# Optimization experiments

Hardware: AMD Instinct MI355X
Metric: run time of the kernel (lower is better)

The kernel has to match this reference:

```python
import jax, jax.numpy as jnp
import numpy as np

DT = 3600.0  # Euler step size (seconds)
N = 2_097_152  # number of timesteps = len(t)


def _get_AB(params):
    """Build the 3x3 A and 3x5 B RC-network matrices from the 7 parameters."""
    Cai, Cwe, Cwi, Re, Ri, Rw, Rg = (params[i] for i in range(7))
    z = jnp.zeros((), params.dtype)
    A = jnp.stack([
        jnp.stack([-1.0 / Cai * (1.0 / Rg + 1.0 / Ri), z, 1.0 / (Cai * Ri)]),
        jnp.stack([z, -1.0 / Cwe * (1.0 / Re + 1.0 / Rw), 1.0 / (Cwe * Rw)]),
        jnp.stack([1.0 / (Cwi * Ri), 1.0 / (Cwi * Rw), -1.0 / Cwi * (1.0 / Rw + 1.0 / Ri)]),
    ])  # [3,3]
    B = jnp.stack([
        jnp.stack([1.0 / (Cai * Rg), 1.0 / Cai, 1.0 / Cai, z, z]),
        jnp.stack([1.0 / (Cwe * Re), z, z, 1.0 / Cwe, z]),
        jnp.stack([z, z, z, z, 1.0 / Cwi]),
    ])  # [3,5]
    return A, B


def setup_inputs() -> dict:
    key = jax.random.key(0)
    d = jax.random.normal(key, (N, 5), dtype=jnp.float32)  # disturbance inputs per step
    params = jnp.array([100000.0, 30000.0, 300000.0, 10.0, 1.0, 10.0, 10.0], dtype=jnp.float32)
    x0 = jnp.array([20.0, 30.0, 26.0], dtype=jnp.float32)  # initial state temps
    return {"params": params, "x0": x0, "d": d}


def reference(params, x0, d):
    # One explicit-Euler step per timestep:
    #   x_{i+1} = x_i + dt*(A x_i + B d_i) = M x_i + c_i,  M = I + dt*A, c_i = dt*B d_i
    A, B = _get_AB(params)
    M = jnp.eye(3, dtype=params.dtype) + DT * A  # [3,3]
    c = DT * (d[:-1] @ B.T)  # [N-1,3]; last row of d is unused (loop runs len(t)-1 steps)

    def step(x, ci):
        xn = M @ x + ci
        return xn, xn

    _, xs = jax.lax.scan(step, x0, c)  # xs: [N-1,3]
    return jnp.concatenate([x0[None, :], xs], axis=0)  # [N,3] == x_all
```

## Files before the change

### kernel.cpp

```cpp
#include <hip/hip_runtime.h>


static constexpr int  N_T   = 2097152;
static constexpr long STEPS = N_T - 1;
static constexpr int  SEG   = 16;
static constexpr int  NSEG  = 131072;
static constexpr int  BLK   = 256;
static constexpr int  NBLK  = NSEG / BLK;

struct Coef {
    float m00,m02,m11,m12,m20,m21,m22;
    float b00,b01,b10,b13,b24;
};

__device__ __forceinline__ Coef derive(const float* __restrict__ p){
    Coef o;
    const float dt = 3600.0f;
    float Cai=p[0],Cwe=p[1],Cwi=p[2],Re=p[3],Ri=p[4],Rw=p[5],Rg=p[6];
    o.m00 = 1.0f + dt * (-1.0f/Cai*(1.0f/Rg + 1.0f/Ri));
    o.m02 = dt * (1.0f/(Cai*Ri));
    o.m11 = 1.0f + dt * (-1.0f/Cwe*(1.0f/Re + 1.0f/Rw));
    o.m12 = dt * (1.0f/(Cwe*Rw));
    o.m20 = dt * (1.0f/(Cwi*Ri));
    o.m21 = dt * (1.0f/(Cwi*Rw));
    o.m22 = 1.0f + dt * (-1.0f/Cwi*(1.0f/Rw + 1.0f/Ri));
    o.b00 = dt * (1.0f/(Cai*Rg));
    o.b01 = dt * (1.0f/Cai);
    o.b10 = dt * (1.0f/(Cwe*Re));
    o.b13 = dt * (1.0f/Cwe);
    o.b24 = dt * (1.0f/Cwi);
    return o;
}

__device__ __forceinline__ void step(const Coef& C, float& s0, float& s1, float& s2,
                                     float d0, float d1, float d2, float d3, float d4){
    float c0 = fmaf(C.b00, d0, C.b01*(d1+d2));
    float c1 = fmaf(C.b10, d0, C.b13*d3);
    float c2 = C.b24*d4;
    float n0 = fmaf(C.m00, s0, fmaf(C.m02, s2, c0));
    float n1 = fmaf(C.m11, s1, fmaf(C.m12, s2, c1));
    float n2 = fmaf(C.m20, s0, fmaf(C.m21, s1, fmaf(C.m22, s2, c2)));
    s0=n0; s1=n1; s2=n2;
}

__device__ __forceinline__ void mm3(const double* X, const double* Y, double* Z){
    #pragma unroll
    for (int r=0;r<3;++r){
        #pragma unroll
        for (int c=0;c<3;++c){
            Z[r*3+c] = X[r*3+0]*Y[0*3+c] + X[r*3+1]*Y[1*3+c] + X[r*3+2]*Y[2*3+c];
        }
    }
}

__device__ __forceinline__ void msq(double* X){
    double T[9]; mm3(X,X,T);
    #pragma unroll
    for (int i=0;i<9;++i) X[i]=T[i];
}

__device__ __forceinline__ void computeM(const float* __restrict__ p, double* Md){
    double Cai=p[0],Cwe=p[1],Cwi=p[2],Re=p[3],Ri=p[4],Rw=p[5],Rg=p[6];
    const double dt = 3600.0;
    Md[0]=1.0 - dt*((1.0/Rg + 1.0/Ri)/Cai); Md[1]=0.0;                              Md[2]=dt/(Cai*Ri);
    Md[3]=0.0;                              Md[4]=1.0 - dt*((1.0/Re + 1.0/Rw)/Cwe); Md[5]=dt/(Cwe*Rw);
    Md[6]=dt/(Cwi*Ri);                      Md[7]=dt/(Cwi*Rw);                      Md[8]=1.0 - dt*((1.0/Rw + 1.0/Ri)/Cwi);
}

__device__ __forceinline__ void lds_scan(float* Ish, int t, int nthr,
                                         double* Qd, float& v0, float& v1, float& v2){
    Ish[t*3+0]=v0; Ish[t*3+1]=v1; Ish[t*3+2]=v2;
    for (int o=1;o<nthr;o<<=1){
        float Qf[9];
        #pragma unroll
        for (int i=0;i<9;++i) Qf[i]=(float)Qd[i];
        __syncthreads();
        float y0=0.f,y1=0.f,y2=0.f;
        if (t>=o){ y0=Ish[(t-o)*3+0]; y1=Ish[(t-o)*3+1]; y2=Ish[(t-o)*3+2]; }
        __syncthreads();
        if (t>=o){
            v0 = Qf[0]*y0+Qf[1]*y1+Qf[2]*y2 + v0;
            v1 = Qf[3]*y0+Qf[4]*y1+Qf[5]*y2 + v1;
            v2 = Qf[6]*y0+Qf[7]*y1+Qf[8]*y2 + v2;
            Ish[t*3+0]=v0; Ish[t*3+1]=v1; Ish[t*3+2]=v2;
        }
        msq(Qd);
    }
    __syncthreads();
}

__global__ __launch_bounds__(256) void k_pass1(const float* __restrict__ d,
                                               const float* __restrict__ p,
                                               float* __restrict__ sArr,
                                               float* __restrict__ blkSum){
    int t = threadIdx.x, b = blockIdx.x;
    int k = b*BLK + t;
    Coef C = derive(p);
    float s0=0.f, s1=0.f, s2=0.f;
    long i0 = (long)k*SEG;
    if (k != NSEG-1){
        const float4* dp = (const float4*)(d + i0*5);
        #pragma unroll
        for (int g=0; g<SEG/4; ++g){
            float4 q0=dp[g*5+0], q1=dp[g*5+1], q2=dp[g*5+2], q3=dp[g*5+3], q4=dp[g*5+4];
            step(C,s0,s1,s2, q0.x,q0.y,q0.z,q0.w,q1.x);
            step(C,s0,s1,s2, q1.y,q1.z,q1.w,q2.x,q2.y);
            step(C,s0,s1,s2, q2.z,q2.w,q3.x,q3.y,q3.z);
            step(C,s0,s1,s2, q3.w,q4.x,q4.y,q4.z,q4.w);
        }
    } else {
        for (long i=i0; i<STEPS; ++i){
            const float* r = d + i*5;
            step(C,s0,s1,s2, r[0],r[1],r[2],r[3],r[4]);
        }
    }
    sArr[k*3+0]=s0; sArr[k*3+1]=s1; sArr[k*3+2]=s2;

    __shared__ float Ish[BLK*3];
    double Pd[9]; computeM(p, Pd);
    msq(Pd); msq(Pd); msq(Pd); msq(Pd);
    double Qd[9];
    #pragma unroll
    for (int i=0;i<9;++i) Qd[i]=Pd[i];
    float v0=s0, v1=s1, v2=s2;
    lds_scan(Ish, t, BLK, Qd, v0, v1, v2);
    if (t==BLK-1){ blkSum[b*3+0]=v0; blkSum[b*3+1]=v1; blkSum[b*3+2]=v2; }
}

__global__ __launch_bounds__(512) void k_pass2(const float* __restrict__ p,
                                               const float* __restrict__ x0,
                                               const float* __restrict__ blkSum,
                                               float* __restrict__ carry){
    __shared__ float Ish[NBLK*3];
    int t = threadIdx.x;
    double Rd[9]; computeM(p, Rd);
    #pragma unroll
    for (int i=0;i<12;++i) msq(Rd);
    float x00=x0[0], x01=x0[1], x02=x0[2];
    float v0=blkSum[t*3+0], v1=blkSum[t*3+1], v2=blkSum[t*3+2];
    if (t==0){
        float Rf[9];
        #pragma unroll
        for (int i=0;i<9;++i) Rf[i]=(float)Rd[i];
        v0 += Rf[0]*x00+Rf[1]*x01+Rf[2]*x02;
        v1 += Rf[3]*x00+Rf[4]*x01+Rf[5]*x02;
        v2 += Rf[6]*x00+Rf[7]*x01+Rf[8]*x02;
    }
    double Qd[9];
    #pragma unroll
    for (int i=0;i<9;++i) Qd[i]=Rd[i];
    lds_scan(Ish, t, NBLK, Qd, v0, v1, v2);
    if (t==0){ carry[0]=x00; carry[1]=x01; carry[2]=x02; }
    else     { carry[t*3+0]=Ish[(t-1)*3+0]; carry[t*3+1]=Ish[(t-1)*3+1]; carry[t*3+2]=Ish[(t-1)*3+2]; }
}

__global__ __launch_bounds__(256) void k_pass3(const float* __restrict__ d,
                                               const float* __restrict__ p,
                                               const float* __restrict__ sArr,
                                               const float* __restrict__ carry,
                                               const float* __restrict__ x0,
                                               float* __restrict__ out){
    int t = threadIdx.x, b = blockIdx.x;
    int k = b*BLK + t;
    Coef C = derive(p);

    __shared__ float Ish[BLK*3];
    double Pd[9]; computeM(p, Pd);
    msq(Pd); msq(Pd); msq(Pd); msq(Pd);
    float U0=carry[b*3+0], U1=carry[b*3+1], U2=carry[b*3+2];
    float v0=sArr[k*3+0], v1=sArr[k*3+1], v2=sArr[k*3+2];
    if (t==0){
        float Pf[9];
        #pragma unroll
        for (int i=0;i<9;++i) Pf[i]=(float)Pd[i];
        v0 += Pf[0]*U0+Pf[1]*U1+Pf[2]*U2;
        v1 += Pf[3]*U0+Pf[4]*U1+Pf[5]*U2;
        v2 += Pf[6]*U0+Pf[7]*U1+Pf[8]*U2;
    }
    double Qd[9];
    #pragma unroll
    for (int i=0;i<9;++i) Qd[i]=Pd[i];
    lds_scan(Ish, t, BLK, Qd, v0, v1, v2);

    float s0,s1,s2;
    if (t==0){ s0=U0; s1=U1; s2=U2; }
    else     { s0=Ish[(t-1)*3+0]; s1=Ish[(t-1)*3+1]; s2=Ish[(t-1)*3+2]; }

    long i0 = (long)k*SEG;
    if (k==0){ out[0]=x0[0]; out[1]=x0[1]; out[2]=x0[2]; }
    if (k != NSEG-1){
        const float4* dp = (const float4*)(d + i0*5);
        float* op = out + (i0+1)*3;
        #pragma unroll
        for (int g=0; g<SEG/4; ++g){
            float4 q0=dp[g*5+0], q1=dp[g*5+1], q2=dp[g*5+2], q3=dp[g*5+3], q4=dp[g*5+4];
            step(C,s0,s1,s2, q0.x,q0.y,q0.z,q0.w,q1.x);
            op[(g*4+0)*3+0]=s0; op[(g*4+0)*3+1]=s1; op[(g*4+0)*3+2]=s2;
            step(C,s0,s1,s2, q1.y,q1.z,q1.w,q2.x,q2.y);
            op[(g*4+1)*3+0]=s0; op[(g*4+1)*3+1]=s1; op[(g*4+1)*3+2]=s2;
            step(C,s0,s1,s2, q2.z,q2.w,q3.x,q3.y,q3.z);
            op[(g*4+2)*3+0]=s0; op[(g*4+2)*3+1]=s1; op[(g*4+2)*3+2]=s2;
            step(C,s0,s1,s2, q3.w,q4.x,q4.y,q4.z,q4.w);
            op[(g*4+3)*3+0]=s0; op[(g*4+3)*3+1]=s1; op[(g*4+3)*3+2]=s2;
        }
    } else {
        for (long i=i0; i<STEPS; ++i){
            const float* r = d + i*5;
            step(C,s0,s1,s2, r[0],r[1],r[2],r[3],r[4]);
            out[(i+1)*3+0]=s0; out[(i+1)*3+1]=s1; out[(i+1)*3+2]=s2;
        }
    }
}

extern "C" void kernel_launch(void* const* d_in, const int* in_sizes, int n_in,
                              void* d_out, int out_size, void* d_ws, size_t ws_size,
                              hipStream_t stream) {
    const float* params = (const float*)d_in[0];
    const float* x0     = (const float*)d_in[1];
    const float* d      = (const float*)d_in[2];
    float* out    = (float*)d_out;
    float* sArr   = (float*)d_ws;
    float* blkSum = sArr + (size_t)NSEG*3;
    float* carry  = blkSum + (size_t)NBLK*3;

    k_pass1<<<NBLK, BLK, 0, stream>>>(d, params, sArr, blkSum);
    k_pass2<<<1, NBLK, 0, stream>>>(params, x0, blkSum, carry);
    k_pass3<<<NBLK, BLK, 0, stream>>>(d, params, sArr, carry, x0, out);
}
```

Before: 49.72 us.

## Restructure linear-recurrence scan into two kernels with recompute and redundant block-prefix

Replaces the three-pass scan (per-segment sums, single-block carry scan, apply) with two kernels. The first computes only block totals through a tree reduction, and no per-segment state is stored. The second has every block redundantly scan all block totals in LDS to get its own carry, then recomputes its segment sums from the input and does the local scan and output. Segment length drops to 8 and the grid grows to 1024 blocks. This removes the single-block middle launch and the workspace round trip, at the cost of reading the input twice plus redundant per-block carry work.

```diff
diff --git a/kernel.cpp b/kernel.cpp
--- a/kernel.cpp
+++ b/kernel.cpp
@@ -1,12 +1,11 @@
 #include <hip/hip_runtime.h>
 
 
-static constexpr int  N_T   = 2097152;
-static constexpr long STEPS = N_T - 1;
-static constexpr int  SEG   = 16;
-static constexpr int  NSEG  = 131072;
-static constexpr int  BLK   = 256;
-static constexpr int  NBLK  = NSEG / BLK;
+static constexpr long STEPS = 2097151;
+static constexpr int  SEG   = 8;
+static constexpr int  TPB   = 256;
+static constexpr int  NBLK  = 1024;
+static constexpr long NSEGT = (long)NBLK*TPB;
 
 struct Coef {
     float m00,m02,m11,m12,m20,m21,m22;
@@ -45,19 +44,14 @@
 
 __device__ __forceinline__ void mm3(const double* X, const double* Y, double* Z){
     #pragma unroll
-    for (int r=0;r<3;++r){
+    for (int r=0;r<3;++r)
         #pragma unroll
-        for (int c=0;c<3;++c){
+        for (int c=0;c<3;++c)
             Z[r*3+c] = X[r*3+0]*Y[0*3+c] + X[r*3+1]*Y[1*3+c] + X[r*3+2]*Y[2*3+c];
-        }
-    }
-}
-
-__device__ __forceinline__ void msq(double* X){
-    double T[9]; mm3(X,X,T);
-    #pragma unroll
-    for (int i=0;i<9;++i) X[i]=T[i];
-}
+}
+__device__ __forceinline__ void msq(double* X){ double T[9]; mm3(X,X,T);
+    #pragma unroll
+    for (int i=0;i<9;++i) X[i]=T[i]; }
 
 __device__ __forceinline__ void computeM(const float* __restrict__ p, double* Md){
     double Cai=p[0],Cwe=p[1],Cwi=p[2],Re=p[3],Ri=p[4],Rw=p[5],Rg=p[6];
@@ -67,148 +61,180 @@
     Md[6]=dt/(Cwi*Ri);                      Md[7]=dt/(Cwi*Rw);                      Md[8]=1.0 - dt*((1.0/Rw + 1.0/Ri)/Cwi);
 }
 
-__device__ __forceinline__ void lds_scan(float* Ish, int t, int nthr,
-                                         double* Qd, float& v0, float& v1, float& v2){
-    Ish[t*3+0]=v0; Ish[t*3+1]=v1; Ish[t*3+2]=v2;
-    for (int o=1;o<nthr;o<<=1){
+__device__ __forceinline__ void seg_sum(const float* __restrict__ d, long i0, const Coef& C,
+                                        float& s0, float& s1, float& s2){
+    const float4* dp = (const float4*)(d + i0*5);
+    s0=0.f; s1=0.f; s2=0.f;
+    #pragma unroll
+    for (int g=0; g<2; ++g){
+        float4 q0=dp[g*5+0], q1=dp[g*5+1], q2=dp[g*5+2], q3=dp[g*5+3], q4=dp[g*5+4];
+        step(C,s0,s1,s2, q0.x,q0.y,q0.z,q0.w,q1.x);
+        step(C,s0,s1,s2, q1.y,q1.z,q1.w,q2.x,q2.y);
+        step(C,s0,s1,s2, q2.z,q2.w,q3.x,q3.y,q3.z);
+        step(C,s0,s1,s2, q3.w,q4.x,q4.y,q4.z,q4.w);
+    }
+}
+
+__global__ __launch_bounds__(256) void k_tot(const float* __restrict__ d,
+                                             const float* __restrict__ p,
+                                             float* __restrict__ blkTot){
+    int t = threadIdx.x, b = blockIdx.x;
+    long k = (long)b*TPB + t;
+    Coef C = derive(p);
+    float s0,s1,s2;
+    seg_sum(d, k*SEG, C, s0,s1,s2);
+
+    __shared__ float a[TPB*3];
+    a[t*3+0]=s0; a[t*3+1]=s1; a[t*3+2]=s2;
+    double Qd[9]; computeM(p, Qd);
+    msq(Qd); msq(Qd); msq(Qd);
+    __syncthreads();
+    for (int off=1; off<TPB; off<<=1){
         float Qf[9];
         #pragma unroll
         for (int i=0;i<9;++i) Qf[i]=(float)Qd[i];
-        __syncthreads();
+        if ((t & (2*off-1))==0){
+            float l0=a[t*3+0], l1=a[t*3+1], l2=a[t*3+2];
+            float r0=a[(t+off)*3+0], r1=a[(t+off)*3+1], r2=a[(t+off)*3+2];
+            a[t*3+0] = r0 + Qf[0]*l0+Qf[1]*l1+Qf[2]*l2;
+            a[t*3+1] = r1 + Qf[3]*l0+Qf[4]*l1+Qf[5]*l2;
+            a[t*3+2] = r2 + Qf[6]*l0+Qf[7]*l1+Qf[8]*l2;
+        }
+        msq(Qd);
+        __syncthreads();
+    }
+    if (t==0){ blkTot[b*3+0]=a[0]; blkTot[b*3+1]=a[1]; blkTot[b*3+2]=a[2]; }
+}
+
+__global__ __launch_bounds__(256) void k_scan(const float* __restrict__ d,
+                                              const float* __restrict__ p,
+                                              const float* __restrict__ blkTot,
+                                              const float* __restrict__ x0,
+                                              float* __restrict__ out){
+    __shared__ float Tl[NBLK*3];
+    __shared__ float Wl[TPB*3];
+    __shared__ float Sl[TPB*3];
+    __shared__ float powA[8][9];
+    __shared__ float powB[8][9];
+    __shared__ float Rm[9];
+
+    int t = threadIdx.x, b = blockIdx.x;
+    long k = (long)b*TPB + t;
+    long i0 = k*SEG;
+    Coef C = derive(p);
+
+    for (int i=t; i<NBLK*3; i+=TPB) Tl[i] = blkTot[i];
+
+    if (t==0){
+        double Qd[9]; computeM(p, Qd);
+        msq(Qd); msq(Qd); msq(Qd);
+        for (int l=0;l<8;++l){
+            #pragma unroll
+            for (int i=0;i<9;++i) powA[l][i]=(float)Qd[i];
+            msq(Qd);
+        }
+        #pragma unroll
+        for (int i=0;i<9;++i) Rm[i]=(float)Qd[i];
+        msq(Qd); msq(Qd);
+        for (int l=0;l<8;++l){
+            #pragma unroll
+            for (int i=0;i<9;++i) powB[l][i]=(float)Qd[i];
+            msq(Qd);
+        }
+    }
+    __syncthreads();
+
+    float x00=x0[0], x01=x0[1], x02=x0[2];
+    if (t==0){
+        Tl[0] += Rm[0]*x00+Rm[1]*x01+Rm[2]*x02;
+        Tl[1] += Rm[3]*x00+Rm[4]*x01+Rm[5]*x02;
+        Tl[2] += Rm[6]*x00+Rm[7]*x01+Rm[8]*x02;
+    }
+    __syncthreads();
+
+    float w0=Tl[(4*t)*3+0], w1=Tl[(4*t)*3+1], w2=Tl[(4*t)*3+2];
+    #pragma unroll
+    for (int j=1;j<4;++j){
+        float n0 = Tl[(4*t+j)*3+0] + Rm[0]*w0+Rm[1]*w1+Rm[2]*w2;
+        float n1 = Tl[(4*t+j)*3+1] + Rm[3]*w0+Rm[4]*w1+Rm[5]*w2;
+        float n2 = Tl[(4*t+j)*3+2] + Rm[6]*w0+Rm[7]*w1+Rm[8]*w2;
+        w0=n0; w1=n1; w2=n2;
+    }
+    Wl[t*3+0]=w0; Wl[t*3+1]=w1; Wl[t*3+2]=w2;
+    __syncthreads();
+    for (int l=0;l<8;++l){
+        int off = 1<<l;
         float y0=0.f,y1=0.f,y2=0.f;
-        if (t>=o){ y0=Ish[(t-o)*3+0]; y1=Ish[(t-o)*3+1]; y2=Ish[(t-o)*3+2]; }
-        __syncthreads();
-        if (t>=o){
-            v0 = Qf[0]*y0+Qf[1]*y1+Qf[2]*y2 + v0;
-            v1 = Qf[3]*y0+Qf[4]*y1+Qf[5]*y2 + v1;
-            v2 = Qf[6]*y0+Qf[7]*y1+Qf[8]*y2 + v2;
-            Ish[t*3+0]=v0; Ish[t*3+1]=v1; Ish[t*3+2]=v2;
-        }
-        msq(Qd);
-    }
-    __syncthreads();
-}
-
-__global__ __launch_bounds__(256) void k_pass1(const float* __restrict__ d,
-                                               const float* __restrict__ p,
-                                               float* __restrict__ sArr,
-                                               float* __restrict__ blkSum){
-    int t = threadIdx.x, b = blockIdx.x;
-    int k = b*BLK + t;
-    Coef C = derive(p);
-    float s0=0.f, s1=0.f, s2=0.f;
-    long i0 = (long)k*SEG;
-    if (k != NSEG-1){
-        const float4* dp = (const float4*)(d + i0*5);
-        #pragma unroll
-        for (int g=0; g<SEG/4; ++g){
-            float4 q0=dp[g*5+0], q1=dp[g*5+1], q2=dp[g*5+2], q3=dp[g*5+3], q4=dp[g*5+4];
-            step(C,s0,s1,s2, q0.x,q0.y,q0.z,q0.w,q1.x);
-            step(C,s0,s1,s2, q1.y,q1.z,q1.w,q2.x,q2.y);
-            step(C,s0,s1,s2, q2.z,q2.w,q3.x,q3.y,q3.z);
-            step(C,s0,s1,s2, q3.w,q4.x,q4.y,q4.z,q4.w);
-        }
-    } else {
-        for (long i=i0; i<STEPS; ++i){
-            const float* r = d + i*5;
-            step(C,s0,s1,s2, r[0],r[1],r[2],r[3],r[4]);
-        }
-    }
-    sArr[k*3+0]=s0; sArr[k*3+1]=s1; sArr[k*3+2]=s2;
-
-    __shared__ float Ish[BLK*3];
-    double Pd[9]; computeM(p, Pd);
-    msq(Pd); msq(Pd); msq(Pd); msq(Pd);
-    double Qd[9];
-    #pragma unroll
-    for (int i=0;i<9;++i) Qd[i]=Pd[i];
+        if (t>=off){ y0=Wl[(t-off)*3+0]; y1=Wl[(t-off)*3+1]; y2=Wl[(t-off)*3+2]; }
+        __syncthreads();
+        if (t>=off){
+            w0 += powB[l][0]*y0+powB[l][1]*y1+powB[l][2]*y2;
+            w1 += powB[l][3]*y0+powB[l][4]*y1+powB[l][5]*y2;
+            w2 += powB[l][6]*y0+powB[l][7]*y1+powB[l][8]*y2;
+            Wl[t*3+0]=w0; Wl[t*3+1]=w1; Wl[t*3+2]=w2;
+        }
+        __syncthreads();
+    }
+
+    float c0,c1,c2;
+    if (b==0){ c0=x00; c1=x01; c2=x02; }
+    else {
+        int e = b-1, q = e>>2;
+        float P0=0.f,P1=0.f,P2=0.f;
+        if (q>0){ P0=Wl[(q-1)*3+0]; P1=Wl[(q-1)*3+1]; P2=Wl[(q-1)*3+2]; }
+        for (int j=4*q; j<=e; ++j){
+            float n0 = Tl[j*3+0] + Rm[0]*P0+Rm[1]*P1+Rm[2]*P2;
+            float n1 = Tl[j*3+1] + Rm[3]*P0+Rm[4]*P1+Rm[5]*P2;
+            float n2 = Tl[j*3+2] + Rm[6]*P0+Rm[7]*P1+Rm[8]*P2;
+            P0=n0; P1=n1; P2=n2;
+        }
+        c0=P0; c1=P1; c2=P2;
+    }
+
+    float s0,s1,s2;
+    seg_sum(d, i0, C, s0,s1,s2);
     float v0=s0, v1=s1, v2=s2;
-    lds_scan(Ish, t, BLK, Qd, v0, v1, v2);
-    if (t==BLK-1){ blkSum[b*3+0]=v0; blkSum[b*3+1]=v1; blkSum[b*3+2]=v2; }
-}
-
-__global__ __launch_bounds__(512) void k_pass2(const float* __restrict__ p,
-                                               const float* __restrict__ x0,
-                                               const float* __restrict__ blkSum,
-                                               float* __restrict__ carry){
-    __shared__ float Ish[NBLK*3];
-    int t = threadIdx.x;
-    double Rd[9]; computeM(p, Rd);
-    #pragma unroll
-    for (int i=0;i<12;++i) msq(Rd);
-    float x00=x0[0], x01=x0[1], x02=x0[2];
-    float v0=blkSum[t*3+0], v1=blkSum[t*3+1], v2=blkSum[t*3+2];
     if (t==0){
-        float Rf[9];
-        #pragma unroll
-        for (int i=0;i<9;++i) Rf[i]=(float)Rd[i];
-        v0 += Rf[0]*x00+Rf[1]*x01+Rf[2]*x02;
-        v1 += Rf[3]*x00+Rf[4]*x01+Rf[5]*x02;
-        v2 += Rf[6]*x00+Rf[7]*x01+Rf[8]*x02;
-    }
-    double Qd[9];
-    #pragma unroll
-    for (int i=0;i<9;++i) Qd[i]=Rd[i];
-    lds_scan(Ish, t, NBLK, Qd, v0, v1, v2);
-    if (t==0){ carry[0]=x00; carry[1]=x01; carry[2]=x02; }
-    else     { carry[t*3+0]=Ish[(t-1)*3+0]; carry[t*3+1]=Ish[(t-1)*3+1]; carry[t*3+2]=Ish[(t-1)*3+2]; }
-}
-
-__global__ __launch_bounds__(256) void k_pass3(const float* __restrict__ d,
-                                               const float* __restrict__ p,
-                                               const float* __restrict__ sArr,
-                                               const float* __restrict__ carry,
-                                               const float* __restrict__ x0,
-                                               float* __restrict__ out){
-    int t = threadIdx.x, b = blockIdx.x;
-    int k = b*BLK + t;
-    Coef C = derive(p);
-
-    __shared__ float Ish[BLK*3];
-    double Pd[9]; computeM(p, Pd);
-    msq(Pd); msq(Pd); msq(Pd); msq(Pd);
-    float U0=carry[b*3+0], U1=carry[b*3+1], U2=carry[b*3+2];
-    float v0=sArr[k*3+0], v1=sArr[k*3+1], v2=sArr[k*3+2];
-    if (t==0){
-        float Pf[9];
-        #pragma unroll
-        for (int i=0;i<9;++i) Pf[i]=(float)Pd[i];
-        v0 += Pf[0]*U0+Pf[1]*U1+Pf[2]*U2;
-        v1 += Pf[3]*U0+Pf[4]*U1+Pf[5]*U2;
-        v2 += Pf[6]*U0+Pf[7]*U1+Pf[8]*U2;
-    }
-    double Qd[9];
-    #pragma unroll
-    for (int i=0;i<9;++i) Qd[i]=Pd[i];
-    lds_scan(Ish, t, BLK, Qd, v0, v1, v2);
-
-    float s0,s1,s2;
-    if (t==0){ s0=U0; s1=U1; s2=U2; }
-    else     { s0=Ish[(t-1)*3+0]; s1=Ish[(t-1)*3+1]; s2=Ish[(t-1)*3+2]; }
-
-    long i0 = (long)k*SEG;
-    if (k==0){ out[0]=x0[0]; out[1]=x0[1]; out[2]=x0[2]; }
-    if (k != NSEG-1){
-        const float4* dp = (const float4*)(d + i0*5);
-        float* op = out + (i0+1)*3;
-        #pragma unroll
-        for (int g=0; g<SEG/4; ++g){
-            float4 q0=dp[g*5+0], q1=dp[g*5+1], q2=dp[g*5+2], q3=dp[g*5+3], q4=dp[g*5+4];
-            step(C,s0,s1,s2, q0.x,q0.y,q0.z,q0.w,q1.x);
-            op[(g*4+0)*3+0]=s0; op[(g*4+0)*3+1]=s1; op[(g*4+0)*3+2]=s2;
-            step(C,s0,s1,s2, q1.y,q1.z,q1.w,q2.x,q2.y);
-            op[(g*4+1)*3+0]=s0; op[(g*4+1)*3+1]=s1; op[(g*4+1)*3+2]=s2;
-            step(C,s0,s1,s2, q2.z,q2.w,q3.x,q3.y,q3.z);
-            op[(g*4+2)*3+0]=s0; op[(g*4+2)*3+1]=s1; op[(g*4+2)*3+2]=s2;
-            step(C,s0,s1,s2, q3.w,q4.x,q4.y,q4.z,q4.w);
-            op[(g*4+3)*3+0]=s0; op[(g*4+3)*3+1]=s1; op[(g*4+3)*3+2]=s2;
-        }
-    } else {
-        for (long i=i0; i<STEPS; ++i){
-            const float* r = d + i*5;
-            step(C,s0,s1,s2, r[0],r[1],r[2],r[3],r[4]);
-            out[(i+1)*3+0]=s0; out[(i+1)*3+1]=s1; out[(i+1)*3+2]=s2;
-        }
+        v0 += powA[0][0]*c0+powA[0][1]*c1+powA[0][2]*c2;
+        v1 += powA[0][3]*c0+powA[0][4]*c1+powA[0][5]*c2;
+        v2 += powA[0][6]*c0+powA[0][7]*c1+powA[0][8]*c2;
+    }
+    Sl[t*3+0]=v0; Sl[t*3+1]=v1; Sl[t*3+2]=v2;
+    __syncthreads();
+    for (int l=0;l<8;++l){
+        int off = 1<<l;
+        float y0=0.f,y1=0.f,y2=0.f;
+        if (t>=off){ y0=Sl[(t-off)*3+0]; y1=Sl[(t-off)*3+1]; y2=Sl[(t-off)*3+2]; }
+        __syncthreads();
+        if (t>=off){
+            v0 += powA[l][0]*y0+powA[l][1]*y1+powA[l][2]*y2;
+            v1 += powA[l][3]*y0+powA[l][4]*y1+powA[l][5]*y2;
+            v2 += powA[l][6]*y0+powA[l][7]*y1+powA[l][8]*y2;
+            Sl[t*3+0]=v0; Sl[t*3+1]=v1; Sl[t*3+2]=v2;
+        }
+        __syncthreads();
+    }
+
+    float g0,g1,g2;
+    if (t==0){ g0=c0; g1=c1; g2=c2; }
+    else     { g0=Sl[(t-1)*3+0]; g1=Sl[(t-1)*3+1]; g2=Sl[(t-1)*3+2]; }
+
+    if (k==0){ out[0]=x00; out[1]=x01; out[2]=x02; }
+    const float4* dp = (const float4*)(d + i0*5);
+    float* op = out + (i0+1)*3;
+    bool full = (k != NSEGT-1);
+    #pragma unroll
+    for (int g=0; g<2; ++g){
+        float4 q0=dp[g*5+0], q1=dp[g*5+1], q2=dp[g*5+2], q3=dp[g*5+3], q4=dp[g*5+4];
+        step(C,g0,g1,g2, q0.x,q0.y,q0.z,q0.w,q1.x);
+        op[(g*4+0)*3+0]=g0; op[(g*4+0)*3+1]=g1; op[(g*4+0)*3+2]=g2;
+        step(C,g0,g1,g2, q1.y,q1.z,q1.w,q2.x,q2.y);
+        op[(g*4+1)*3+0]=g0; op[(g*4+1)*3+1]=g1; op[(g*4+1)*3+2]=g2;
+        step(C,g0,g1,g2, q2.z,q2.w,q3.x,q3.y,q3.z);
+        op[(g*4+2)*3+0]=g0; op[(g*4+2)*3+1]=g1; op[(g*4+2)*3+2]=g2;
+        step(C,g0,g1,g2, q3.w,q4.x,q4.y,q4.z,q4.w);
+        if (g==1 && !full) break;
+        op[(g*4+3)*3+0]=g0; op[(g*4+3)*3+1]=g1; op[(g*4+3)*3+2]=g2;
     }
 }
 
@@ -219,11 +245,8 @@
     const float* x0     = (const float*)d_in[1];
     const float* d      = (const float*)d_in[2];
     float* out    = (float*)d_out;
-    float* sArr   = (float*)d_ws;
-    float* blkSum = sArr + (size_t)NSEG*3;
-    float* carry  = blkSum + (size_t)NBLK*3;
-
-    k_pass1<<<NBLK, BLK, 0, stream>>>(d, params, sArr, blkSum);
-    k_pass2<<<1, NBLK, 0, stream>>>(params, x0, blkSum, carry);
-    k_pass3<<<NBLK, BLK, 0, stream>>>(d, params, sArr, carry, x0, out);
-}
+    float* blkTot = (float*)d_ws;
+
+    k_tot <<<NBLK, TPB, 0, stream>>>(d, params, blkTot);
+    k_scan<<<NBLK, TPB, 0, stream>>>(d, params, blkTot, x0, out);
+}
```

Measured after the change: 45.84 us. 7.8% less time.
